# Optimization experiments

Hardware: AMD Instinct MI355X
Metric: run time of the kernel (lower is better)

## Reference

```python
import jax, jax.numpy as jnp
import numpy as np

B, LQ, LK, D, H, DK, DV = 8, 1024, 1024, 512, 8, 64, 64
EPS = 1e-14          # K.epsilon()**2 with default K.epsilon()=1e-7
MASK_VALUE = -1e30   # default mask_value in call()


def setup_inputs() -> dict:
    key = jax.random.key(0)
    ks = jax.random.split(key, 7)
    query = jax.random.normal(ks[0], (B, LQ, D), jnp.float32)
    key_t = jax.random.normal(ks[1], (B, LK, D), jnp.float32)
    value = jax.random.normal(ks[2], (B, LK, D), jnp.float32)
    mask = jax.random.randint(ks[3], (B, LK), 0, 2).astype(jnp.float32)
    glorot = np.sqrt(2.0 / (D + DK)).astype(np.float32)
    Wq = jax.random.normal(ks[4], (H, D, DK), jnp.float32) * glorot
    Wk = jax.random.normal(ks[5], (H, D, DK), jnp.float32) * glorot
    Wv = jax.random.normal(ks[6], (H, D, DV), jnp.float32) * glorot
    gamma = jnp.ones((1,), jnp.float32)
    beta = jnp.zeros((1,), jnp.float32)
    return {"query": query, "key": key_t, "value": value, "mask": mask,
            "Wq": Wq, "Wk": Wk, "Wv": Wv, "gamma": gamma, "beta": beta}


def reference(query, key, value, mask, Wq, Wk, Wv, gamma, beta):
    # Per-head projections (the original's Python loop over heads, vectorized).
    q = jnp.einsum('bqd,hde->bhqe', query, Wq)   # [B,H,LQ,DK]
    k = jnp.einsum('bkd,hde->bhke', key, Wk)     # [B,H,LK,DK]
    v = jnp.einsum('bkd,hde->bhke', value, Wv)   # [B,H,LK,DV]
    # NOTE: no 1/sqrt(dk) scaling, faithful to the source.
    A = jnp.einsum('bhqe,bhke->bhqk', q, k)      # [B,H,LQ,LK]
    m = mask[:, None, None, :]                    # [B,1,1,LK] broadcast over heads & queries
    A = m * A + (1.0 - m) * MASK_VALUE
    A = jax.nn.softmax(A, axis=-1)
    o = jnp.einsum('bhqk,bhke->bhqe', A, v)      # [B,H,LQ,DV]
    conc = o.transpose(0, 2, 1, 3).reshape(B, LQ, H * DV)  # concat heads
    # Scalar-affine layernorm over the concatenated feature dim.
    mean = jnp.mean(conc, axis=-1, keepdims=True)
    var = jnp.mean(jnp.square(conc - mean), axis=-1, keepdims=True)
    x = (conc - mean) / jnp.sqrt(var + EPS)
    return x * gamma[0] + beta[0]
```

## Files before the change

### kernel.cpp

```cpp
#include <hip/hip_runtime.h>
#include <math.h>

#define NB 8
#define NLQ 1024
#define NLK 1024
#define ND 512
#define NH 8
#define MASKV -1e30f
#define LOG2E 1.44269504088896f
#define SHIFT2 32.0f

typedef unsigned short ushort_t;
typedef __attribute__((ext_vector_type(8))) _Float16 f16x8;
typedef __attribute__((ext_vector_type(8))) short bf16x8;
typedef __attribute__((ext_vector_type(16))) float f32x16;

__device__ __forceinline__ ushort_t f2h_bits(float f) {
    union { _Float16 h; ushort_t u; } v; v.h = (_Float16)f;
    return v.u;
}
__device__ __forceinline__ ushort_t f2bf(float f) {
    union { float f; unsigned u; } v; v.f = f;
    unsigned r = v.u + 0x7fffu + ((v.u >> 16) & 1u);
    return (ushort_t)(r >> 16);
}
__device__ __forceinline__ void gload16(const ushort_t* g, ushort_t* l) {
    __builtin_amdgcn_global_load_lds(
        (const __attribute__((address_space(1))) void*)g,
        (__attribute__((address_space(3))) void*)l, 16, 0, 0);
}
__device__ __forceinline__ unsigned pack_bf16_trunc(float p0, float p1) {
    return __builtin_amdgcn_perm(__float_as_uint(p1), __float_as_uint(p0),
                                 0x07060302u);
}

__global__ __launch_bounds__(256) void wsplit_kernel(
    const float* __restrict__ Wq, const float* __restrict__ Wk, const float* __restrict__ Wv,
    ushort_t* __restrict__ oq, ushort_t* __restrict__ ok, ushort_t* __restrict__ ov) {
    __shared__ float T[64][65];
    const int d0 = blockIdx.x * 64;
    const int h  = blockIdx.y;
    const int t  = blockIdx.z;
    const float* W = (t == 0) ? Wq : (t == 1) ? Wk : Wv;
    ushort_t* oh = (t == 0) ? oq : (t == 1) ? ok : ov;
    const int tid = threadIdx.x;
#pragma unroll
    for (int i = 0; i < 4; i++) {
        int r = (tid >> 4) + i * 16;
        int c = (tid & 15) * 4;
        float4 v = *(const float4*)&W[((size_t)h * ND + d0 + r) * 64 + c];
        *(float4*)&T[r][c] = v;
    }
    __syncthreads();
    const int e = tid & 63;
    const int dg = tid >> 6;
    ushort_t hs[16];
#pragma unroll
    for (int dd = 0; dd < 16; dd++) hs[dd] = f2h_bits(T[dg * 16 + dd][e]);
    size_t base = ((size_t)h * 64 + e) * ND + d0 + dg * 16;
#pragma unroll
    for (int c = 0; c < 2; c++) {
        uint4 wh;
        wh.x = (unsigned)hs[8*c+0] | ((unsigned)hs[8*c+1] << 16);
        wh.y = (unsigned)hs[8*c+2] | ((unsigned)hs[8*c+3] << 16);
        wh.z = (unsigned)hs[8*c+4] | ((unsigned)hs[8*c+5] << 16);
        wh.w = (unsigned)hs[8*c+6] | ((unsigned)hs[8*c+7] << 16);
        *(uint4*)&oh[base + 8 * c] = wh;
    }
}

__global__ __launch_bounds__(256, 4) void proj_mfma_kernel(
    const float* __restrict__ Xq, const float* __restrict__ Xk,
    const float* __restrict__ Xv, const ushort_t* __restrict__ Wbase,
    ushort_t* __restrict__ Obase) {
    __shared__ ushort_t sX[2][4160];
    __shared__ ushort_t sW[2][4160];

    const int l0 = blockIdx.x * 64;
    const int h  = blockIdx.y;
    const int z  = blockIdx.z;
    const int t  = z >> 3;
    const int b  = z & 7;
    const int tid  = threadIdx.x;
    const int wave = tid >> 6;
    const int lane = tid & 63;
    const int l31  = lane & 31;
    const int hib  = lane >> 5;
    const size_t bh = (size_t)b * NH + h;

    const float* Xt = (t == 0) ? Xq : (t == 1) ? Xk : Xv;
    const float* gx = Xt + ((size_t)b * NLQ + l0) * ND;
    const ushort_t* gw = Wbase + (size_t)t * ((size_t)NH * 64 * ND)
                       + (size_t)h * 64 * ND;
    ushort_t* out = Obase + (size_t)t * ((size_t)NB * NH * NLQ * 64);

    const int srow = lane >> 3;
    const int schk = (lane & 7) ^ srow;

    float4 lx[2][2];
    auto xload = [&](int d0) {
#pragma unroll
        for (int i = 0; i < 2; i++) {
            int u = i * 4 + wave;
            int row = u * 8 + srow;
            const float* p = gx + (size_t)row * ND + d0 + schk * 8;
            lx[i][0] = *(const float4*)p;
            lx[i][1] = *(const float4*)(p + 4);
        }
    };
    auto xwrite = [&](int buf) {
#pragma unroll
        for (int i = 0; i < 2; i++) {
            int u = i * 4 + wave;
            uint4 hv;
            hv.x = (unsigned)f2h_bits(lx[i][0].x) | ((unsigned)f2h_bits(lx[i][0].y) << 16);
            hv.y = (unsigned)f2h_bits(lx[i][0].z) | ((unsigned)f2h_bits(lx[i][0].w) << 16);
            hv.z = (unsigned)f2h_bits(lx[i][1].x) | ((unsigned)f2h_bits(lx[i][1].y) << 16);
            hv.w = (unsigned)f2h_bits(lx[i][1].z) | ((unsigned)f2h_bits(lx[i][1].w) << 16);
            *(uint4*)(sX[buf] + u * 520 + lane * 8) = hv;
        }
    };
    auto wstage = [&](int buf, int d0) {
#pragma unroll
        for (int i = 0; i < 2; i++) {
            int u = i * 4 + wave;
            int row = u * 8 + srow;
            gload16(gw + (size_t)row * ND + d0 + schk * 8, sW[buf] + u * 520);
        }
    };

    f32x16 acc;
#pragma unroll
    for (int i = 0; i < 16; i++) acc[i] = 0.f;

    const int arow = (wave >> 1) * 32 + l31;
    const int brow = (wave & 1) * 32 + l31;
    const int apad = (arow >> 3) * 520 + (arow & 7) * 64;
    const int bpad = (brow >> 3) * 520 + (brow & 7) * 64;
    const int sw = l31 & 7;

    xload(0);
    wstage(0, 0);
    xwrite(0);
    __syncthreads();
    int cur = 0;
    for (int kc = 0; kc < 8; kc++) {
        if (kc < 7) {
            xload((kc + 1) * 64);
            wstage(cur ^ 1, (kc + 1) * 64);
        }
#pragma unroll
        for (int c = 0; c < 4; c++) {
            const int pc = ((2 * c + hib) ^ sw) * 8;
            f16x8 xh = *(const f16x8*)&sX[cur][apad + pc];
            f16x8 wh = *(const f16x8*)&sW[cur][bpad + pc];
            acc = __builtin_amdgcn_mfma_f32_32x32x16_f16(xh, wh, acc, 0, 0, 0);
        }
        if (kc < 7) xwrite(cur ^ 1);
        __syncthreads();
        cur ^= 1;
    }

    if (t < 2) {
        const float scale = (t == 0) ? LOG2E : 1.f;
        const size_t obase = (bh * NLQ + l0) * 64;
        const int e = (wave & 1) * 32 + l31;
#pragma unroll
        for (int r = 0; r < 16; r++) {
            int l = (wave >> 1) * 32 + (r & 3) + 8 * (r >> 2) + 4 * hib;
            out[obase + (size_t)l * 64 + e] = f2h_bits(acc[r] * scale);
        }
    } else {
        ushort_t (*T)[68] = (ushort_t(*)[68])sX;
        const int e = (wave & 1) * 32 + l31;
#pragma unroll
        for (int r = 0; r < 16; r++) {
            int l = (wave >> 1) * 32 + (r & 3) + 8 * (r >> 2) + 4 * hib;
            T[e][l] = f2bf(acc[r]);
        }
        __syncthreads();
        const int e2 = tid >> 2;
        const int lc = (tid & 3) * 16;
        size_t base = (bh * 64 + e2) * NLK + l0 + lc;
        *(uint4*)&out[base]     = *(const uint4*)&T[e2][lc];
        *(uint4*)&out[base + 8] = *(const uint4*)&T[e2][lc + 8];
    }
}

__global__ __launch_bounds__(256, 4) void attn_kernel(
    const ushort_t* __restrict__ Qf, const ushort_t* __restrict__ Kf,
    const ushort_t* __restrict__ Vt, const float* __restrict__ maskp,
    float* __restrict__ Op) {
    __shared__ ushort_t sK[2][4160];
    __shared__ ushort_t sV[2][4160];
    __shared__ float sBias[1024];

    const int idx = blockIdx.x;
    const int bh_i = idx & 63;
    const int qc  = idx >> 6;
    const int b = bh_i >> 3, h = bh_i & 7;
    const size_t bh = (size_t)b * NH + h;

    const int tid  = threadIdx.x;
    const int wave = tid >> 6;
    const int lane = tid & 63;
    const int l31  = lane & 31;
    const int hib  = lane >> 5;
    const int q = qc * 128 + wave * 32 + l31;
    const int sw = l31 & 7;

    {
        const float* mrow = maskp + ((size_t)b << 10);
        float4 m0 = *(const float4*)&mrow[tid * 4];
        float4 bi;
        bi.x = (m0.x > 0.5f) ? -SHIFT2 : MASKV;
        bi.y = (m0.y > 0.5f) ? -SHIFT2 : MASKV;
        bi.z = (m0.z > 0.5f) ? -SHIFT2 : MASKV;
        bi.w = (m0.w > 0.5f) ? -SHIFT2 : MASKV;
        *(float4*)&sBias[tid * 4] = bi;
    }

    f16x8 qh[4];
    {
        const ushort_t* ph = Qf + (bh * NLQ + q) * 64 + hib * 8;
#pragma unroll
        for (int c = 0; c < 4; c++) qh[c] = *(const f16x8*)(ph + c * 16);
    }

    const int srow = lane >> 3;
    const int schk = (lane & 7) ^ srow;

    auto stage = [&](int buf, int k0) {
#pragma unroll
        for (int n = 0; n < 4; n++) {
            int u = wave + n * 4;
            if (u < 8) {
                int row = u * 8 + srow;
                int key = (row & ~12) | ((row & 4) << 1) | ((row & 8) >> 1);
                gload16(Kf + ((bh << 10) + k0 + key) * 64 + schk * 8,
                        sK[buf] + u * 520);
            } else {
                int u8 = u - 8;
                int row = u8 * 8 + srow;
                gload16(Vt + ((bh << 6) + row) * NLK + k0 + schk * 8,
                        sV[buf] + u8 * 520);
            }
        }
    };

    f32x16 O0, O1;
#pragma unroll
    for (int i = 0; i < 16; i++) { O0[i] = 0.f; O1[i] = 0.f; }
    float lrun = 0.f;

    const int rp0 = (l31 >> 3) * 520 + (l31 & 7) * 64;
    const int rp1 = rp0 + 4 * 520;

    stage(0, 0);
    __syncthreads();
    int cur = 0;

    for (int t = 0; t < 16; t++) {
        const int k0 = t << 6;
        if (t < 15) stage(cur ^ 1, k0 + 64);

        f32x16 S0, S1;
#pragma unroll
        for (int g = 0; g < 4; g++) {
            const int kb = k0 + 16 * (g >> 1) + 8 * hib + 4 * (g & 1);
            float4 b0 = *(const float4*)&sBias[kb];
            float4 b1 = *(const float4*)&sBias[kb + 32];
            S0[4 * g + 0] = b0.x; S0[4 * g + 1] = b0.y;
            S0[4 * g + 2] = b0.z; S0[4 * g + 3] = b0.w;
            S1[4 * g + 0] = b1.x; S1[4 * g + 1] = b1.y;
            S1[4 * g + 2] = b1.z; S1[4 * g + 3] = b1.w;
        }
#pragma unroll
        for (int c = 0; c < 4; c++) {
            const int pc = ((2 * c + hib) ^ sw) * 8;
            f16x8 a0 = *(const f16x8*)&sK[cur][rp0 + pc];
            f16x8 a1 = *(const f16x8*)&sK[cur][rp1 + pc];
            S0 = __builtin_amdgcn_mfma_f32_32x32x16_f16(a0, qh[c], S0, 0, 0, 0);
            S1 = __builtin_amdgcn_mfma_f32_32x32x16_f16(a1, qh[c], S1, 0, 0, 0);
        }

        unsigned pq[8][2];
#pragma unroll
        for (int g = 0; g < 8; g++) {
            float p0, p1, p2, p3;
            if (g < 4) {
                p0 = __builtin_amdgcn_exp2f(S0[4*g+0]);
                p1 = __builtin_amdgcn_exp2f(S0[4*g+1]);
                p2 = __builtin_amdgcn_exp2f(S0[4*g+2]);
                p3 = __builtin_amdgcn_exp2f(S0[4*g+3]);
            } else {
                p0 = __builtin_amdgcn_exp2f(S1[4*(g-4)+0]);
                p1 = __builtin_amdgcn_exp2f(S1[4*(g-4)+1]);
                p2 = __builtin_amdgcn_exp2f(S1[4*(g-4)+2]);
                p3 = __builtin_amdgcn_exp2f(S1[4*(g-4)+3]);
            }
            lrun += (p0 + p1) + (p2 + p3);
            pq[g][0] = pack_bf16_trunc(p0, p1);
            pq[g][1] = pack_bf16_trunc(p2, p3);
        }

#pragma unroll
        for (int c = 0; c < 4; c++) {
            union { unsigned u[4]; bf16x8 v; } pf;
            pf.u[0] = pq[2 * c][0];     pf.u[1] = pq[2 * c][1];
            pf.u[2] = pq[2 * c + 1][0]; pf.u[3] = pq[2 * c + 1][1];
            const int pc = ((2 * c + hib) ^ sw) * 8;
            bf16x8 v0 = *(const bf16x8*)&sV[cur][rp0 + pc];
            bf16x8 v1 = *(const bf16x8*)&sV[cur][rp1 + pc];
            O0 = __builtin_amdgcn_mfma_f32_32x32x16_bf16(v0, pf.v, O0, 0, 0, 0);
            O1 = __builtin_amdgcn_mfma_f32_32x32x16_bf16(v1, pf.v, O1, 0, 0, 0);
        }
        __syncthreads();
        cur ^= 1;
    }

    lrun += __shfl_xor(lrun, 32);
    const float linv = 1.f / lrun;
    float* obase = Op + ((size_t)(b * NLQ + q)) * (NH * 64) + h * 64;
#pragma unroll
    for (int me = 0; me < 2; me++) {
#pragma unroll
        for (int g = 0; g < 4; g++) {
            int e0 = me * 32 + 8 * g + 4 * hib;
            float4 o;
            if (me == 0) {
                o.x = O0[4 * g + 0] * linv; o.y = O0[4 * g + 1] * linv;
                o.z = O0[4 * g + 2] * linv; o.w = O0[4 * g + 3] * linv;
            } else {
                o.x = O1[4 * g + 0] * linv; o.y = O1[4 * g + 1] * linv;
                o.z = O1[4 * g + 2] * linv; o.w = O1[4 * g + 3] * linv;
            }
            *(float4*)&obase[e0] = o;
        }
    }
}

__global__ __launch_bounds__(256) void ln_kernel(const float* __restrict__ X,
                                                 const float* __restrict__ gamma,
                                                 const float* __restrict__ beta,
                                                 float* __restrict__ out) {
    const int row = blockIdx.x * 4 + (threadIdx.x >> 6);
    const int lane = threadIdx.x & 63;
    const float* x = &X[(size_t)row * 512];
    float4 v0 = *(const float4*)&x[lane * 8];
    float4 v1 = *(const float4*)&x[lane * 8 + 4];
    float sum = v0.x + v0.y + v0.z + v0.w + v1.x + v1.y + v1.z + v1.w;
    float sq = v0.x * v0.x + v0.y * v0.y + v0.z * v0.z + v0.w * v0.w
             + v1.x * v1.x + v1.y * v1.y + v1.z * v1.z + v1.w * v1.w;
#pragma unroll
    for (int off = 32; off > 0; off >>= 1) {
        sum += __shfl_down(sum, off);
        sq  += __shfl_down(sq, off);
    }
    sum = __shfl(sum, 0);
    sq  = __shfl(sq, 0);
    const float mean = sum * (1.f / 512.f);
    const float var = sq * (1.f / 512.f) - mean * mean;
    const float rstd = rsqrtf(var + 1e-14f);
    const float g = gamma[0], be = beta[0];
    float* o = &out[(size_t)row * 512];
    float4 r0, r1;
    r0.x = (v0.x - mean) * rstd * g + be;  r0.y = (v0.y - mean) * rstd * g + be;
    r0.z = (v0.z - mean) * rstd * g + be;  r0.w = (v0.w - mean) * rstd * g + be;
    r1.x = (v1.x - mean) * rstd * g + be;  r1.y = (v1.y - mean) * rstd * g + be;
    r1.z = (v1.z - mean) * rstd * g + be;  r1.w = (v1.w - mean) * rstd * g + be;
    *(float4*)&o[lane * 8] = r0;
    *(float4*)&o[lane * 8 + 4] = r1;
}

extern "C" void kernel_launch(void* const* d_in, const int* in_sizes, int n_in,
                              void* d_out, int out_size, void* d_ws, size_t ws_size,
                              hipStream_t stream) {
    const float* query = (const float*)d_in[0];
    const float* key_t = (const float*)d_in[1];
    const float* value = (const float*)d_in[2];
    const float* mask  = (const float*)d_in[3];
    const float* Wq    = (const float*)d_in[4];
    const float* Wk    = (const float*)d_in[5];
    const float* Wv    = (const float*)d_in[6];
    const float* gamma = (const float*)d_in[7];
    const float* beta  = (const float*)d_in[8];
    float* out = (float*)d_out;

    const size_t A = (size_t)NB * NLQ * ND;
    const size_t WS = (size_t)NH * 64 * ND;
    ushort_t* Qf = (ushort_t*)d_ws;
    ushort_t* Kf = Qf + A;
    ushort_t* Vt = Qf + 2 * A;
    ushort_t* Wt = Qf + 3 * A;

    wsplit_kernel<<<dim3(ND / 64, NH, 3), 256, 0, stream>>>(
        Wq, Wk, Wv, Wt, Wt + WS, Wt + 2 * WS);

    proj_mfma_kernel<<<dim3(NLQ / 64, NH, 24), 256, 0, stream>>>(
        query, key_t, value, Wt, Qf);

    attn_kernel<<<512, 256, 0, stream>>>(Qf, Kf, Vt, mask, out);

    ln_kernel<<<(NB * NLQ) / 4, 256, 0, stream>>>(out, gamma, beta, out);
}
```

Measured before the change: 169.8 us.

## Deepen projection GEMM prefetch to two stages and stage weights through registers

The projection GEMM loop now keeps two register sets of global loads in flight, issuing loads two K-chunks ahead. The weight tile is read into registers and written to shared memory alongside the activation tile, replacing the previous direct global-to-LDS copy. The K loop is fully unrolled with fixed buffer indices and precomputed row pointers, which removes address arithmetic. This aims to hide global memory latency better, at the cost of more registers and possibly lower occupancy.

```diff
diff --git a/kernel.cpp b/kernel.cpp
--- a/kernel.cpp
+++ b/kernel.cpp
@@ -97,37 +97,38 @@
     const int srow = lane >> 3;
     const int schk = (lane & 7) ^ srow;
 
-    float4 lx[2][2];
-    auto xload = [&](int d0) {
-#pragma unroll
-        for (int i = 0; i < 2; i++) {
-            int u = i * 4 + wave;
-            int row = u * 8 + srow;
-            const float* p = gx + (size_t)row * ND + d0 + schk * 8;
-            lx[i][0] = *(const float4*)p;
-            lx[i][1] = *(const float4*)(p + 4);
-        }
-    };
-    auto xwrite = [&](int buf) {
-#pragma unroll
-        for (int i = 0; i < 2; i++) {
-            int u = i * 4 + wave;
-            uint4 hv;
-            hv.x = (unsigned)f2h_bits(lx[i][0].x) | ((unsigned)f2h_bits(lx[i][0].y) << 16);
-            hv.y = (unsigned)f2h_bits(lx[i][0].z) | ((unsigned)f2h_bits(lx[i][0].w) << 16);
-            hv.z = (unsigned)f2h_bits(lx[i][1].x) | ((unsigned)f2h_bits(lx[i][1].y) << 16);
-            hv.w = (unsigned)f2h_bits(lx[i][1].z) | ((unsigned)f2h_bits(lx[i][1].w) << 16);
-            *(uint4*)(sX[buf] + u * 520 + lane * 8) = hv;
-        }
-    };
-    auto wstage = [&](int buf, int d0) {
-#pragma unroll
-        for (int i = 0; i < 2; i++) {
-            int u = i * 4 + wave;
-            int row = u * 8 + srow;
-            gload16(gw + (size_t)row * ND + d0 + schk * 8, sW[buf] + u * 520);
-        }
-    };
+    const float*    gx0 = gx + (size_t)(wave * 8 + srow) * ND + schk * 8;
+    const float*    gx1 = gx0 + (size_t)32 * ND;
+    const ushort_t* gw0 = gw + (size_t)(wave * 8 + srow) * ND + schk * 8;
+    const ushort_t* gw1 = gw0 + (size_t)32 * ND;
+
+    float4 xA[2][2], xB[2][2];
+    uint4  wA[2],  wB[2];
+
+#define LOADSET(xs, ws, d0) do {                                   \
+        xs[0][0] = *(const float4*)(gx0 + (d0));                    \
+        xs[0][1] = *(const float4*)(gx0 + (d0) + 4);                \
+        xs[1][0] = *(const float4*)(gx1 + (d0));                    \
+        xs[1][1] = *(const float4*)(gx1 + (d0) + 4);                \
+        ws[0]    = *(const uint4*)(gw0 + (d0));                     \
+        ws[1]    = *(const uint4*)(gw1 + (d0));                     \
+    } while (0)
+
+#define WRITESET(buf, xs, ws) do {                                              \
+        uint4 hv0, hv1;                                                          \
+        hv0.x = (unsigned)f2h_bits(xs[0][0].x) | ((unsigned)f2h_bits(xs[0][0].y) << 16); \
+        hv0.y = (unsigned)f2h_bits(xs[0][0].z) | ((unsigned)f2h_bits(xs[0][0].w) << 16); \
+        hv0.z = (unsigned)f2h_bits(xs[0][1].x) | ((unsigned)f2h_bits(xs[0][1].y) << 16); \
+        hv0.w = (unsigned)f2h_bits(xs[0][1].z) | ((unsigned)f2h_bits(xs[0][1].w) << 16); \
+        hv1.x = (unsigned)f2h_bits(xs[1][0].x) | ((unsigned)f2h_bits(xs[1][0].y) << 16); \
+        hv1.y = (unsigned)f2h_bits(xs[1][0].z) | ((unsigned)f2h_bits(xs[1][0].w) << 16); \
+        hv1.z = (unsigned)f2h_bits(xs[1][1].x) | ((unsigned)f2h_bits(xs[1][1].y) << 16); \
+        hv1.w = (unsigned)f2h_bits(xs[1][1].z) | ((unsigned)f2h_bits(xs[1][1].w) << 16); \
+        *(uint4*)(sX[buf] + wave * 520 + lane * 8)            = hv0;             \
+        *(uint4*)(sX[buf] + (4 + wave) * 520 + lane * 8)      = hv1;             \
+        *(uint4*)(sW[buf] + wave * 520 + lane * 8)            = ws[0];           \
+        *(uint4*)(sW[buf] + (4 + wave) * 520 + lane * 8)      = ws[1];           \
+    } while (0)
 
     f32x16 acc;
 #pragma unroll
@@ -139,27 +140,36 @@
     const int bpad = (brow >> 3) * 520 + (brow & 7) * 64;
     const int sw = l31 & 7;
 
-    xload(0);
-    wstage(0, 0);
-    xwrite(0);
+#define MFMA4(buf) do {                                             \
+        _Pragma("unroll")                                            \
+        for (int c = 0; c < 4; c++) {                                \
+            const int pc = ((2 * c + hib) ^ sw) * 8;                 \
+            f16x8 xh = *(const f16x8*)&sX[buf][apad + pc];           \
+            f16x8 wh = *(const f16x8*)&sW[buf][bpad + pc];           \
+            acc = __builtin_amdgcn_mfma_f32_32x32x16_f16(xh, wh, acc, 0, 0, 0); \
+        }                                                            \
+    } while (0)
+
+    LOADSET(xA, wA, 0);
+    LOADSET(xB, wB, 64);
+    WRITESET(0, xA, wA);
     __syncthreads();
-    int cur = 0;
-    for (int kc = 0; kc < 8; kc++) {
-        if (kc < 7) {
-            xload((kc + 1) * 64);
-            wstage(cur ^ 1, (kc + 1) * 64);
-        }
-#pragma unroll
-        for (int c = 0; c < 4; c++) {
-            const int pc = ((2 * c + hib) ^ sw) * 8;
-            f16x8 xh = *(const f16x8*)&sX[cur][apad + pc];
-            f16x8 wh = *(const f16x8*)&sW[cur][bpad + pc];
-            acc = __builtin_amdgcn_mfma_f32_32x32x16_f16(xh, wh, acc, 0, 0, 0);
-        }
-        if (kc < 7) xwrite(cur ^ 1);
+
+#pragma unroll
+    for (int kc = 0; kc < 8; kc += 2) {
+        if (kc + 2 < 8) LOADSET(xA, wA, (kc + 2) * 64);
+        WRITESET(1, xB, wB);
+        MFMA4(0);
         __syncthreads();
-        cur ^= 1;
-    }
+        if (kc + 3 < 8) LOADSET(xB, wB, (kc + 3) * 64);
+        if (kc + 2 < 8) WRITESET(0, xA, wA);
+        MFMA4(1);
+        __syncthreads();
+    }
+
+#undef LOADSET
+#undef WRITESET
+#undef MFMA4
 
     if (t < 2) {
         const float scale = (t == 0) ? LOG2E : 1.f;
```

New measurement: 211.1 us. 24.3% more time.

## Stage fp32 activations directly to LDS with async loads in projection kernel

Applied to the files above, without the earlier changes.

The projection kernel now copies the fp32 X tiles straight into shared memory with global_load_lds, using an XOR-swizzled layout, instead of loading them into registers, converting to fp16 and writing to LDS. The fp16 conversion moves to the point where MFMA operands are read from LDS. Manual vmcnt waits and raw s_barriers replace __syncthreads so the next stage's loads stay in flight during the MFMA loop. In exchange, LDS usage roughly doubles for the X buffers, occupancy drops to 3 blocks per CU, each K-step repeats the conversions, and correctness now rests on the hand-written wait counts.

```diff
diff --git a/kernel.cpp b/kernel.cpp
--- a/kernel.cpp
+++ b/kernel.cpp
@@ -25,6 +25,11 @@
     return (ushort_t)(r >> 16);
 }
 __device__ __forceinline__ void gload16(const ushort_t* g, ushort_t* l) {
+    __builtin_amdgcn_global_load_lds(
+        (const __attribute__((address_space(1))) void*)g,
+        (__attribute__((address_space(3))) void*)l, 16, 0, 0);
+}
+__device__ __forceinline__ void gload16f(const float* g, float* l) {
     __builtin_amdgcn_global_load_lds(
         (const __attribute__((address_space(1))) void*)g,
         (__attribute__((address_space(3))) void*)l, 16, 0, 0);
@@ -69,12 +74,12 @@
     }
 }
 
-__global__ __launch_bounds__(256, 4) void proj_mfma_kernel(
+__global__ __launch_bounds__(256, 3) void proj_mfma_kernel(
     const float* __restrict__ Xq, const float* __restrict__ Xk,
     const float* __restrict__ Xv, const ushort_t* __restrict__ Wbase,
     ushort_t* __restrict__ Obase) {
-    __shared__ ushort_t sX[2][4160];
-    __shared__ ushort_t sW[2][4160];
+    __shared__ float    sXf[2][4160];
+    __shared__ ushort_t sW [2][4160];
 
     const int l0 = blockIdx.x * 64;
     const int h  = blockIdx.y;
@@ -96,31 +101,17 @@
 
     const int srow = lane >> 3;
     const int schk = (lane & 7) ^ srow;
-
-    float4 lx[2][2];
-    auto xload = [&](int d0) {
-#pragma unroll
-        for (int i = 0; i < 2; i++) {
-            int u = i * 4 + wave;
-            int row = u * 8 + srow;
-            const float* p = gx + (size_t)row * ND + d0 + schk * 8;
-            lx[i][0] = *(const float4*)p;
-            lx[i][1] = *(const float4*)(p + 4);
-        }
-    };
-    auto xwrite = [&](int buf) {
-#pragma unroll
-        for (int i = 0; i < 2; i++) {
-            int u = i * 4 + wave;
-            uint4 hv;
-            hv.x = (unsigned)f2h_bits(lx[i][0].x) | ((unsigned)f2h_bits(lx[i][0].y) << 16);
-            hv.y = (unsigned)f2h_bits(lx[i][0].z) | ((unsigned)f2h_bits(lx[i][0].w) << 16);
-            hv.z = (unsigned)f2h_bits(lx[i][1].x) | ((unsigned)f2h_bits(lx[i][1].y) << 16);
-            hv.w = (unsigned)f2h_bits(lx[i][1].z) | ((unsigned)f2h_bits(lx[i][1].w) << 16);
-            *(uint4*)(sX[buf] + u * 520 + lane * 8) = hv;
-        }
-    };
-    auto wstage = [&](int buf, int d0) {
+    const int xrow = lane >> 4;
+    const int xc16 = lane & 15;
+
+    auto stage = [&](int buf, int d0) {
+#pragma unroll
+        for (int j = 0; j < 4; j++) {
+            int s = j * 4 + wave;
+            int row = s * 4 + xrow;
+            int c16 = xc16 ^ ((row & 7) << 1);
+            gload16f(gx + (size_t)row * ND + d0 + c16 * 4, sXf[buf] + s * 260);
+        }
 #pragma unroll
         for (int i = 0; i < 2; i++) {
             int u = i * 4 + wave;
@@ -133,31 +124,44 @@
 #pragma unroll
     for (int i = 0; i < 16; i++) acc[i] = 0.f;
 
-    const int arow = (wave >> 1) * 32 + l31;
-    const int brow = (wave & 1) * 32 + l31;
-    const int apad = (arow >> 3) * 520 + (arow & 7) * 64;
-    const int bpad = (brow >> 3) * 520 + (brow & 7) * 64;
-    const int sw = l31 & 7;
-
-    xload(0);
-    wstage(0, 0);
-    xwrite(0);
-    __syncthreads();
+    const int arow  = (wave >> 1) * 32 + l31;
+    const int brow  = (wave & 1) * 32 + l31;
+    const int xbase = (arow >> 2) * 260 + (arow & 3) * 64;
+    const int sxz   = (arow & 7) << 1;
+    const int bpad  = (brow >> 3) * 520 + (brow & 7) * 64;
+    const int sw    = l31 & 7;
+
+    stage(0, 0);
     int cur = 0;
+#pragma unroll
     for (int kc = 0; kc < 8; kc++) {
         if (kc < 7) {
-            xload((kc + 1) * 64);
-            wstage(cur ^ 1, (kc + 1) * 64);
-        }
+            stage(cur ^ 1, (kc + 1) * 64);
+            asm volatile("s_waitcnt vmcnt(6)" ::: "memory");
+        } else {
+            asm volatile("s_waitcnt vmcnt(0)" ::: "memory");
+        }
+        __builtin_amdgcn_sched_barrier(0);
+        __builtin_amdgcn_s_barrier();
+        __builtin_amdgcn_sched_barrier(0);
 #pragma unroll
         for (int c = 0; c < 4; c++) {
+            const int sl = ((2 * c + hib) * 2) ^ sxz;
+            const float* xp = &sXf[cur][xbase + sl * 4];
+            float4 fa = *(const float4*)xp;
+            float4 fb = *(const float4*)(xp + 4);
+            f16x8 xh;
+            xh[0] = (_Float16)fa.x; xh[1] = (_Float16)fa.y;
+            xh[2] = (_Float16)fa.z; xh[3] = (_Float16)fa.w;
+            xh[4] = (_Float16)fb.x; xh[5] = (_Float16)fb.y;
+            xh[6] = (_Float16)fb.z; xh[7] = (_Float16)fb.w;
             const int pc = ((2 * c + hib) ^ sw) * 8;
-            f16x8 xh = *(const f16x8*)&sX[cur][apad + pc];
             f16x8 wh = *(const f16x8*)&sW[cur][bpad + pc];
             acc = __builtin_amdgcn_mfma_f32_32x32x16_f16(xh, wh, acc, 0, 0, 0);
         }
-        if (kc < 7) xwrite(cur ^ 1);
-        __syncthreads();
+        __builtin_amdgcn_sched_barrier(0);
+        __builtin_amdgcn_s_barrier();
+        __builtin_amdgcn_sched_barrier(0);
         cur ^= 1;
     }
 
@@ -171,7 +175,7 @@
             out[obase + (size_t)l * 64 + e] = f2h_bits(acc[r] * scale);
         }
     } else {
-        ushort_t (*T)[68] = (ushort_t(*)[68])sX;
+        ushort_t (*T)[68] = (ushort_t(*)[68])sXf;
         const int e = (wave & 1) * 32 + l31;
 #pragma unroll
         for (int r = 0; r < 16; r++) {
```

New measurement: 184.9 us. 1.09x slower.
